# Performance work log

Measured on AMD Instinct MI355X. Metric: run time of the kernel, lower is better.

The kernel has to match this reference:

```python
import jax, jax.numpy as jnp
import numpy as np

HEADS = 4
DIM_HEAD = 32
SCALE = DIM_HEAD ** -0.5

# Energy conventions (Hopfield / Lagrangian formulation):
#  Neuron(x): g = activation(x); e = sum(x*g) - L(x)
#  Synapse(g, x): e = -sum(g*x)
#  identity Lagrangian: L(x) = 0.5*sum(x^2), g = x  => Conv2d block energy = -0.5*sum(x^2)
#  softmax Lagrangian: L(x) = sum(logsumexp(x, -1)), g = softmax(x, -1)

def setup_inputs() -> dict:
    key = jax.random.key(0)
    ks = jax.random.split(key, 5)
    b, c, h, w = 8, 256, 48, 48
    hidden = HEADS * DIM_HEAD  # 128
    return {
        "x": jax.random.normal(ks[0], (b, c, h, w), jnp.float32),
        "w_qkv": jax.random.normal(ks[1], (hidden * 3, c), jnp.float32) * 0.02,
        "b_qkv": jax.random.normal(ks[2], (hidden * 3,), jnp.float32) * 0.02,
        "w_out": jax.random.normal(ks[3], (c, hidden), jnp.float32) * 0.02,
        "b_out": jax.random.normal(ks[4], (c,), jnp.float32) * 0.02,
    }

def reference(x, w_qkv, b_qkv, w_out, b_out):
    b, c, h, w = x.shape
    # 1x1 conv == channel matmul
    qkv = jnp.einsum('oc,bcxy->boxy', w_qkv, x) + b_qkv[None, :, None, None]
    e_qkv = -0.5 * jnp.sum(qkv * qkv)  # identity-Lagrangian neuron + synapse energy
    q, k, v = jnp.split(qkv, 3, axis=1)
    # 'b (h c) x y -> b h c (x y)'
    def heads(t):
        return t.reshape(b, HEADS, DIM_HEAD, h * w)
    q, k, v = heads(q), heads(k), heads(v)
    q = q * SCALE
    sim = jnp.einsum('bhdi,bhdj->bhij', q, k)  # [b, heads, hw, hw]
    sim = sim - jax.lax.stop_gradient(jnp.max(sim, axis=-1, keepdims=True))
    attn = jax.nn.softmax(sim, axis=-1)
    # softmax-Lagrangian neuron energy: sum(sim*attn) - sum(logsumexp(sim, -1))
    e_attn = jnp.sum(sim * attn) - jnp.sum(jax.nn.logsumexp(sim, axis=-1))
    out = jnp.einsum('bhij,bhdj->bhid', attn, v)  # [b, heads, hw, dim_head]
    # 'b h (x y) d -> b (h d) x y'
    out = out.transpose(0, 1, 3, 2).reshape(b, HEADS * DIM_HEAD, h, w)
    out = jnp.einsum('oc,bcxy->boxy', w_out, out) + b_out[None, :, None, None]
    e_out = -0.5 * jnp.sum(out * out)
    return out, e_attn + e_out + e_qkv
```

## Files before the change

kernel.cpp:

```cpp
#include <hip/hip_runtime.h>
#include <hip/hip_bf16.h>

#define HW 2304
#define HW2 4608
#define NB 8
#define NC 256
#define HID 128
#define DH 32
#define NH 4
#define SCALE 0.17677669529663687f
#define LOG2E 1.4426950408889634f
#define LN2   0.6931471805599453f

#define NSPLIT 4
#define OSZ ((size_t)NB * HW * HID)

using bf16x8 = __attribute__((ext_vector_type(8))) short;
using f32x4  = __attribute__((ext_vector_type(4))) float;

__device__ __forceinline__ short f2bf(float f) {
    unsigned u = __float_as_uint(f);
    u += 0x7FFF + ((u >> 16) & 1);
    return (short)(u >> 16);
}
__device__ __forceinline__ float bf2f(short s) {
    return __uint_as_float(((unsigned)(unsigned short)s) << 16);
}
__device__ __forceinline__ unsigned pk2bf(float a, float b) {
    union { __hip_bfloat162 h; unsigned u; } cv;
    cv.h = __float22bfloat162_rn(float2{a, b});
    return cv.u;
}
__device__ __forceinline__ void gld16(const void* g, void* l) {
    __builtin_amdgcn_global_load_lds(
        (const __attribute__((address_space(1))) unsigned*)g,
        (__attribute__((address_space(3))) unsigned*)l, 16, 0, 0);
}
#define SB() __builtin_amdgcn_sched_barrier(0)

__global__ __launch_bounds__(256)
void prep(const float* __restrict__ x, const float* __restrict__ wq,
          const float* __restrict__ wo, short* __restrict__ Xt,
          short* __restrict__ Wq, short* __restrict__ Wo, float* __restrict__ wsz)
{
    if (blockIdx.z == 8) {
        const int bid = blockIdx.x + 36 * blockIdx.y;
        if (bid == 0 && threadIdx.x == 0) { wsz[0] = 0.f; ((int*)wsz)[1] = 0; }
        for (int i = bid * 256 + threadIdx.x; i < 384 * 256; i += 144 * 256) {
            Wq[i] = f2bf(wq[i]);
            if (i < 256 * 128) Wo[i] = f2bf(wo[i]);
        }
        return;
    }
    __shared__ short Tb[64][72];
    const int b = blockIdx.z, c0 = blockIdx.y * 64, s0 = blockIdx.x * 64;
    const int ts4 = (threadIdx.x & 15) * 4;
    const int cc0 = threadIdx.x >> 4;
    #pragma unroll
    for (int pp = 0; pp < 4; ++pp) {
        const int cc = cc0 + pp * 16;
        const float4 v = *(const float4*)(
            x + ((size_t)b * NC + c0 + cc) * HW + s0 + ts4);
        Tb[ts4 + 0][cc] = f2bf(v.x);
        Tb[ts4 + 1][cc] = f2bf(v.y);
        Tb[ts4 + 2][cc] = f2bf(v.z);
        Tb[ts4 + 3][cc] = f2bf(v.w);
    }
    __syncthreads();
    const int ss = threadIdx.x >> 2;
    const int c8 = (threadIdx.x & 3) * 8;
    #pragma unroll
    for (int pp = 0; pp < 2; ++pp) {
        const int cc = c8 + pp * 32;
        const bf16x8 v = *(const bf16x8*)&Tb[ss][cc];
        *(bf16x8*)(Xt + ((size_t)b * HW + s0 + ss) * NC + c0 + cc) = v;
    }
}

__global__ __launch_bounds__(256, 2)
void conv_qkv(const short* __restrict__ A, const short* __restrict__ Bt,
              const float* __restrict__ bias,
              short* __restrict__ Qb, short* __restrict__ Kb,
              short* __restrict__ Kt, short* __restrict__ Vb,
              float* __restrict__ E)
{
    constexpr int KD = NC;
    constexpr int NI = KD / 32;
    const int b  = blockIdx.z;
    const int bm = blockIdx.y * 64;
    const int bn = blockIdx.x * 128;
    const int t  = threadIdx.x;
    const int w  = t >> 6, lane = t & 63;
    const int n16 = lane & 15, quad = lane >> 4;

    __shared__ __align__(16) char csm[4 * 12288];
    __shared__ float red[4];

    const int rL = lane >> 2, cswz = (lane & 3) ^ (rL & 3);
    const char* agl = (const char*)(A  + (size_t)(bm + rL) * KD + cswz * 8);
    const char* bgl = (const char*)(Bt + ((size_t)b * HW + bn + rL) * KD + cswz * 8);

    auto issue = [&](int kc, int pbuf) {
        char* base = csm + pbuf * 12288;
        if (w == 0) {
            gld16(agl + (size_t)(0 * 16 * KD + kc) * 2, base + 0 * 1024);
            gld16(agl + (size_t)(1 * 16 * KD + kc) * 2, base + 1 * 1024);
            gld16(bgl + (size_t)(0 * 16 * KD + kc) * 2, base + 4096 + 0 * 1024);
        } else if (w == 1) {
            gld16(agl + (size_t)(2 * 16 * KD + kc) * 2, base + 2 * 1024);
            gld16(agl + (size_t)(3 * 16 * KD + kc) * 2, base + 3 * 1024);
            gld16(bgl + (size_t)(1 * 16 * KD + kc) * 2, base + 4096 + 1 * 1024);
        } else if (w == 2) {
            gld16(bgl + (size_t)(2 * 16 * KD + kc) * 2, base + 4096 + 2 * 1024);
            gld16(bgl + (size_t)(3 * 16 * KD + kc) * 2, base + 4096 + 3 * 1024);
            gld16(bgl + (size_t)(4 * 16 * KD + kc) * 2, base + 4096 + 4 * 1024);
        } else {
            gld16(bgl + (size_t)(5 * 16 * KD + kc) * 2, base + 4096 + 5 * 1024);
            gld16(bgl + (size_t)(6 * 16 * KD + kc) * 2, base + 4096 + 6 * 1024);
            gld16(bgl + (size_t)(7 * 16 * KD + kc) * 2, base + 4096 + 7 * 1024);
        }
    };

    f32x4 acc[4][2] = {};
    const int rsw = (quad ^ (n16 & 3)) * 16;

    issue(0, 0); SB();
    issue(32, 1); SB();
    for (int ki = 0; ki < NI; ++ki) {
        if (ki + 2 < NI) {
            issue((ki + 2) * 32, (ki + 2) & 3);
            asm volatile("s_waitcnt vmcnt(6)" ::: "memory");
        } else if (ki + 2 == NI) {
            asm volatile("s_waitcnt vmcnt(3)" ::: "memory");
        } else {
            asm volatile("s_waitcnt vmcnt(0)" ::: "memory");
        }
        __builtin_amdgcn_s_barrier();
        SB();

        const char* Ap = csm + (ki & 3) * 12288;
        const char* Bp = Ap + 4096;
        bf16x8 am[4], bq[2];
        #pragma unroll
        for (int tm = 0; tm < 4; ++tm)
            am[tm] = *(const bf16x8*)(Ap + tm * 1024 + n16 * 64 + rsw);
        #pragma unroll
        for (int j = 0; j < 2; ++j)
            bq[j] = *(const bf16x8*)(Bp + (w * 2 + j) * 1024 + n16 * 64 + rsw);
        #pragma unroll
        for (int tm = 0; tm < 4; ++tm)
            #pragma unroll
            for (int j = 0; j < 2; ++j)
                acc[tm][j] = __builtin_amdgcn_mfma_f32_16x16x32_bf16(am[tm], bq[j], acc[tm][j], 0, 0, 0);
    }

    float e = 0.f;
    #pragma unroll
    for (int tm = 0; tm < 4; ++tm) {
        const int o0 = bm + tm * 16 + quad * 4;
        const float4 bb = *(const float4*)(bias + o0);
        #pragma unroll
        for (int j = 0; j < 2; ++j) {
            const int s = bn + (w * 2 + j) * 16 + n16;
            float v[4] = {acc[tm][j][0] + bb.x, acc[tm][j][1] + bb.y,
                          acc[tm][j][2] + bb.z, acc[tm][j][3] + bb.w};
            e -= 0.5f * (v[0]*v[0] + v[1]*v[1] + v[2]*v[2] + v[3]*v[3]);
            if (o0 < HID) {
                const int h = o0 >> 5, dh0 = o0 & 31;
                const float qs = SCALE * LOG2E;
                short4 pk = {f2bf(v[0]*qs), f2bf(v[1]*qs),
                             f2bf(v[2]*qs), f2bf(v[3]*qs)};
                *(short4*)(Qb + ((size_t)(b * NH + h) * HW + s) * DH + dh0) = pk;
            } else if (o0 < 2 * HID) {
                const int c = o0 - HID, h = c >> 5, dh0 = c & 31;
                const int g = s & 31;
                const int sp = (s & ~31) | ((g & 4) << 2) | ((g >> 3) << 2) | (g & 3);
                short4 pk = {f2bf(v[0]), f2bf(v[1]), f2bf(v[2]), f2bf(v[3])};
                *(short4*)(Kb + ((size_t)(b * NH + h) * HW + sp) * DH + dh0) = pk;
                #pragma unroll
                for (int r = 0; r < 4; ++r)
                    Kt[((size_t)(b * NH + h) * DH + dh0 + r) * HW + s] = f2bf(v[r]);
            } else {
                const int c = o0 - 2 * HID, h = c >> 5, dh0 = c & 31;
                #pragma unroll
                for (int r = 0; r < 4; ++r)
                    Vb[((size_t)(b * NH + h) * DH + dh0 + r) * HW + s] = f2bf(v[r]);
            }
        }
    }

    #pragma unroll
    for (int off = 32; off > 0; off >>= 1) e += __shfl_down(e, off);
    if (lane == 0) red[w] = e;
    __syncthreads();
    if (t == 0) atomicAdd(E, red[0] + red[1] + red[2] + red[3]);
}

__global__ __launch_bounds__(256)
void flashsplit(const short* __restrict__ Qb, const short* __restrict__ Kb,
                const short* __restrict__ Kt, const short* __restrict__ Vb,
                short* __restrict__ Oh, float* __restrict__ lsP,
                float* __restrict__ tsP)
{
    __shared__ __align__(16) char smem[2 * 12288];

    constexpr int ITERS = HW / (NSPLIT * 64);
    const int bh   = blockIdx.y;
    const int kh   = blockIdx.z;
    const int w    = threadIdx.x >> 6;
    const int lane = threadIdx.x & 63;
    const int n16  = lane & 15, quad = lane >> 4;
    const int qb   = blockIdx.x * 128 + w * 32;
    const int key0 = kh * ITERS * 64;

    bf16x8 aq[2];
    #pragma unroll
    for (int qg = 0; qg < 2; ++qg)
        aq[qg] = *(const bf16x8*)(Qb + ((size_t)bh * HW + qb + qg * 16 + n16) * DH + quad * 8);
    SB();

    const int rL = lane >> 2, cL = (lane & 3) ^ (rL & 3);
    const char* Kglb  = (const char*)(Kb + (size_t)bh * HW * DH);
    const char* Vglb  = (const char*)(Vb + (size_t)bh * DH * HW);
    const char* Ktglb = (const char*)(Kt + (size_t)bh * DH * HW);
    const int pca  = w & 1;
    const int ktca = w >> 1;
    const int ktu  = w & 1;

    auto stage = [&](int it, int pbuf) {
        char* buf = smem + pbuf * 12288;
        const int k64 = key0 + it * 64;
        if (w < 2) {
            const char* kg = Kglb + (size_t)(k64 + pca * 32 + rL) * 64 + cL * 16;
            gld16(kg,        buf + pca * 6144 + 0);
            gld16(kg + 1024, buf + pca * 6144 + 1024);
        } else {
            const char* vg = Vglb + (size_t)rL * HW2 + (size_t)(k64 + pca * 32) * 2 + cL * 16;
            gld16(vg,             buf + pca * 6144 + 2048);
            gld16(vg + 16 * HW2,  buf + pca * 6144 + 3072);
        }
        const char* kt = Ktglb + (size_t)(ktu * 16 + rL) * HW2
                       + (size_t)(k64 + ktca * 32) * 2 + cL * 16;
        gld16(kt, buf + ktca * 6144 + 4096 + ktu * 1024);
    };

    stage(0, 0);
    SB();

    f32x4 acc[2][2] = {};
    f32x4 lsacc[2] = {};
    f32x4 tsacc[2][2] = {};
    const int swz = (quad ^ (n16 & 3)) * 8;
    const bf16x8 ones = {0x3F80, 0x3F80, 0x3F80, 0x3F80,
                         0x3F80, 0x3F80, 0x3F80, 0x3F80};

    for (int it = 0; it < ITERS; ++it) {
        const int p = it & 1;
        asm volatile("s_waitcnt vmcnt(0)" ::: "memory");
        __builtin_amdgcn_s_barrier();
        SB();
        if (it + 1 < ITERS) stage(it + 1, p ^ 1);

        const char* buf = smem + p * 12288;
        #pragma unroll
        for (int ca = 0; ca < 2; ++ca) {
            const short* cb = (const short*)(buf + ca * 6144);

            const bf16x8 bk0  = *(const bf16x8*)(cb +        n16 * 32 + swz);
            const bf16x8 bk1  = *(const bf16x8*)(cb + 512  + n16 * 32 + swz);
            const bf16x8 bv0  = *(const bf16x8*)(cb + 1024 + n16 * 32 + swz);
            const bf16x8 bv1  = *(const bf16x8*)(cb + 1536 + n16 * 32 + swz);
            const bf16x8 bkt0 = *(const bf16x8*)(cb + 2048 + n16 * 32 + swz);
            const bf16x8 bkt1 = *(const bf16x8*)(cb + 2560 + n16 * 32 + swz);

            #pragma unroll
            for (int qg = 0; qg < 2; ++qg) {
                f32x4 z = {};
                const f32x4 s0 = __builtin_amdgcn_mfma_f32_16x16x32_bf16(bk0, aq[qg], z, 0, 0, 0);
                const f32x4 s1 = __builtin_amdgcn_mfma_f32_16x16x32_bf16(bk1, aq[qg], z, 0, 0, 0);
                float e0[4], e1[4];
                #pragma unroll
                for (int r = 0; r < 4; ++r) {
                    e0[r] = __builtin_amdgcn_exp2f(s0[r]);
                    e1[r] = __builtin_amdgcn_exp2f(s1[r]);
                }
                union { bf16x8 v; unsigned u[4]; } pa;
                pa.u[0] = pk2bf(e0[0], e0[1]);
                pa.u[1] = pk2bf(e0[2], e0[3]);
                pa.u[2] = pk2bf(e1[0], e1[1]);
                pa.u[3] = pk2bf(e1[2], e1[3]);
                acc[qg][0]   = __builtin_amdgcn_mfma_f32_16x16x32_bf16(bv0,  pa.v, acc[qg][0], 0, 0, 0);
                acc[qg][1]   = __builtin_amdgcn_mfma_f32_16x16x32_bf16(bv1,  pa.v, acc[qg][1], 0, 0, 0);
                lsacc[qg]    = __builtin_amdgcn_mfma_f32_16x16x32_bf16(ones, pa.v, lsacc[qg], 0, 0, 0);
                tsacc[qg][0] = __builtin_amdgcn_mfma_f32_16x16x32_bf16(bkt0, pa.v, tsacc[qg][0], 0, 0, 0);
                tsacc[qg][1] = __builtin_amdgcn_mfma_f32_16x16x32_bf16(bkt1, pa.v, tsacc[qg][1], 0, 0, 0);
            }
        }
    }

    const int bb = bh >> 2, h = bh & 3;
    short* dst = Oh + (size_t)kh * OSZ;
    #pragma unroll
    for (int qg = 0; qg < 2; ++qg) {
        const int q = qb + qg * 16 + n16;
        const float L = lsacc[qg][0];
        const short4 qa = *(const short4*)(Qb + ((size_t)bh * HW + q) * DH + quad * 4);
        const short4 qc = *(const short4*)(Qb + ((size_t)bh * HW + q) * DH + 16 + quad * 4);
        float ts = bf2f(qa.x) * tsacc[qg][0][0] + bf2f(qa.y) * tsacc[qg][0][1]
                 + bf2f(qa.z) * tsacc[qg][0][2] + bf2f(qa.w) * tsacc[qg][0][3]
                 + bf2f(qc.x) * tsacc[qg][1][0] + bf2f(qc.y) * tsacc[qg][1][1]
                 + bf2f(qc.z) * tsacc[qg][1][2] + bf2f(qc.w) * tsacc[qg][1][3];
        ts += __shfl_xor(ts, 16);
        ts += __shfl_xor(ts, 32);

        const float invl = 1.f / L;
        short* ap = dst + ((size_t)bb * HW + q) * HID + h * 32;
        short4 pk0 = {f2bf(acc[qg][0][0] * invl), f2bf(acc[qg][0][1] * invl),
                      f2bf(acc[qg][0][2] * invl), f2bf(acc[qg][0][3] * invl)};
        short4 pk1 = {f2bf(acc[qg][1][0] * invl), f2bf(acc[qg][1][1] * invl),
                      f2bf(acc[qg][1][2] * invl), f2bf(acc[qg][1][3] * invl)};
        *(short4*)(ap + quad * 4)      = pk0;
        *(short4*)(ap + 16 + quad * 4) = pk1;
        if (quad == 0) {
            const size_t li = (size_t)(kh * 32 + bh) * HW + q;
            lsP[li] = L;
            tsP[li] = ts;
        }
    }
}

__global__ __launch_bounds__(256, 2)
void conv_out(const short* __restrict__ A, const short* __restrict__ Oh,
              const float* __restrict__ lsP, const float* __restrict__ tsP,
              const float* __restrict__ bias, float* __restrict__ out0,
              float* __restrict__ E, int* __restrict__ ticket, int nblocks,
              float* __restrict__ edst)
{
    constexpr int KD = HID;
    constexpr int NI = KD / 32;
    const int b  = blockIdx.z;
    const int bm = blockIdx.y * 64;
    const int bn = blockIdx.x * 128;
    const int t  = threadIdx.x;
    const int w  = t >> 6, lane = t & 63;
    const int n16 = lane & 15, quad = lane >> 4;

    __shared__ __align__(16) char csm[24576];
    __shared__ float red[4];

    const int rL = lane >> 2, cswz = (lane & 3) ^ (rL & 3);
    const char* agl = (const char*)(A + (size_t)(bm + rL) * KD + cswz * 8);

    auto issueA = [&](int kc, int pbuf) {
        char* base = csm + pbuf * 12288;
        if (w == 0) {
            gld16(agl + (size_t)(0 * 16 * KD + kc) * 2, base + 0 * 1024);
            gld16(agl + (size_t)(1 * 16 * KD + kc) * 2, base + 1 * 1024);
        } else if (w == 1) {
            gld16(agl + (size_t)(2 * 16 * KD + kc) * 2, base + 2 * 1024);
            gld16(agl + (size_t)(3 * 16 * KD + kc) * 2, base + 3 * 1024);
        }
    };

    auto loadB = [&](int ki, bf16x8 pk[2]) {
        const int kc = ki * 32;
        const int bh = b * NH + ki;
        #pragma unroll
        for (int d = 0; d < 2; ++d) {
            const int blk = w * 2 + d;
            const int q = bn + blk * 16 + rL;
            float Ls[NSPLIT], sum = 0.f;
            #pragma unroll
            for (int kh = 0; kh < NSPLIT; ++kh) {
                Ls[kh] = lsP[(size_t)(kh * 32 + bh) * HW + q];
                sum += Ls[kh];
            }
            const float inv = 1.f / sum;
            float vv[8] = {};
            #pragma unroll
            for (int kh = 0; kh < NSPLIT; ++kh) {
                const float wk = Ls[kh] * inv;
                const bf16x8 o = *(const bf16x8*)(Oh + (size_t)kh * OSZ
                                    + ((size_t)b * HW + q) * HID + kc + cswz * 8);
                #pragma unroll
                for (int j = 0; j < 8; ++j) vv[j] += wk * bf2f(o[j]);
            }
            union { bf16x8 v; unsigned u[4]; } c;
            #pragma unroll
            for (int i = 0; i < 4; ++i) c.u[i] = pk2bf(vv[2*i], vv[2*i+1]);
            pk[d] = c.v;
        }
    };
    auto writeB = [&](const bf16x8 pk[2], int pbuf) {
        char* base = csm + pbuf * 12288 + 4096;
        #pragma unroll
        for (int d = 0; d < 2; ++d) {
            const int blk = w * 2 + d;
            *(bf16x8*)(base + blk * 1024 + rL * 64 + (lane & 3) * 16) = pk[d];
        }
    };

    f32x4 acc[4][2] = {};
    const int rsw = (quad ^ (n16 & 3)) * 16;

    bf16x8 bpk[2];
    loadB(0, bpk);
    issueA(0, 0);
    writeB(bpk, 0);
    for (int ki = 0; ki < NI; ++ki) {
        const int p = ki & 1;
        __syncthreads();
        if (ki + 1 < NI) { loadB(ki + 1, bpk); issueA((ki + 1) * 32, p ^ 1); }

        const char* Ap = csm + p * 12288;
        const char* Bp = Ap + 4096;
        bf16x8 am[4], bq[2];
        #pragma unroll
        for (int tm = 0; tm < 4; ++tm)
            am[tm] = *(const bf16x8*)(Ap + tm * 1024 + n16 * 64 + rsw);
        #pragma unroll
        for (int j = 0; j < 2; ++j)
            bq[j] = *(const bf16x8*)(Bp + (w * 2 + j) * 1024 + n16 * 64 + rsw);
        #pragma unroll
        for (int tm = 0; tm < 4; ++tm)
            #pragma unroll
            for (int j = 0; j < 2; ++j)
                acc[tm][j] = __builtin_amdgcn_mfma_f32_16x16x32_bf16(am[tm], bq[j], acc[tm][j], 0, 0, 0);

        if (ki + 1 < NI) writeB(bpk, p ^ 1);
    }

    float e = 0.f;
    #pragma unroll
    for (int tm = 0; tm < 4; ++tm) {
        const int o0 = bm + tm * 16 + quad * 4;
        const float4 bb = *(const float4*)(bias + o0);
        #pragma unroll
        for (int j = 0; j < 2; ++j) {
            const int s = bn + (w * 2 + j) * 16 + n16;
            float v[4] = {acc[tm][j][0] + bb.x, acc[tm][j][1] + bb.y,
                          acc[tm][j][2] + bb.z, acc[tm][j][3] + bb.w};
            e -= 0.5f * (v[0]*v[0] + v[1]*v[1] + v[2]*v[2] + v[3]*v[3]);
            #pragma unroll
            for (int r = 0; r < 4; ++r)
                out0[((size_t)b * NC + o0 + r) * HW + s] = v[r];
        }
    }

    if (blockIdx.y == 0) {
        const int q = bn + (t & 127);
        #pragma unroll
        for (int jj = 0; jj < 2; ++jj) {
            const int h = (t >> 7) * 2 + jj;
            const int bh = b * NH + h;
            float L = 0.f, T = 0.f;
            #pragma unroll
            for (int kh = 0; kh < NSPLIT; ++kh) {
                L += lsP[(size_t)(kh * 32 + bh) * HW + q];
                T += tsP[(size_t)(kh * 32 + bh) * HW + q];
            }
            e += (LN2 * T) / L - __logf(L);
        }
    }

    #pragma unroll
    for (int off = 32; off > 0; off >>= 1) e += __shfl_down(e, off);
    if (lane == 0) red[w] = e;
    __syncthreads();
    if (t == 0) {
        atomicAdd(E, red[0] + red[1] + red[2] + red[3]);
        __threadfence();
        const int prev = atomicAdd(ticket, 1);
        if (prev == nblocks - 1) {
            __threadfence();
            edst[0] = atomicAdd(E, 0.f);
        }
    }
}

extern "C" void kernel_launch(void* const* d_in, const int* in_sizes, int n_in,
                              void* d_out, int out_size, void* d_ws, size_t ws_size,
                              hipStream_t stream) {
    const float* x     = (const float*)d_in[0];
    const float* w_qkv = (const float*)d_in[1];
    const float* b_qkv = (const float*)d_in[2];
    const float* w_out = (const float*)d_in[3];
    const float* b_out = (const float*)d_in[4];
    float* out = (float*)d_out;

    float* wsf    = (float*)d_ws;
    float* E      = wsf;
    int*   ticket = (int*)d_ws + 1;
    short* Xt   = (short*)(wsf + 16);
    short* Wq   = Xt + (size_t)NB * HW * NC;
    short* Wo   = Wq + 384 * 256;
    short* Qb   = Wo + 256 * 128;
    short* Kb   = Qb + (size_t)NB * NH * HW * DH;
    short* Ktb  = Kb + (size_t)NB * NH * HW * DH;
    short* Vb   = Ktb + (size_t)NB * NH * HW * DH;
    short* Oh   = Vb + (size_t)NB * NH * HW * DH;
    float* lsP  = (float*)(Oh + NSPLIT * OSZ);
    float* tsP  = lsP + NSPLIT * 32 * HW;

    prep<<<dim3(HW / 64, NC / 64, NB + 1), 256, 0, stream>>>(
        x, w_qkv, w_out, Xt, Wq, Wo, wsf);
    conv_qkv<<<dim3(18, 6, NB), 256, 0, stream>>>(
        Wq, Xt, b_qkv, Qb, Kb, Ktb, Vb, E);
    flashsplit<<<dim3(HW / 128, NB * NH, NSPLIT), 256, 0, stream>>>(
        Qb, Kb, Ktb, Vb, Oh, lsP, tsP);
    conv_out<<<dim3(18, 4, NB), 256, 0, stream>>>(
        Wo, Oh, lsP, tsP, b_out, out, E, ticket, 18 * 4 * NB,
        out + (size_t)NB * NC * HW);
}
```

Measured before the change: 192.9 us.

## Double-buffer 64-wide K chunks in QKV conv and remap flash blocks per XCD

The QKV projection kernel now stages 64-channel K chunks into two large shared buffers, replacing the four-deep 32-channel ring with finer vmcnt waits. It waits for all loads, then prefetches the next chunk after the barrier, giving fewer loop iterations and barriers in exchange for coarser overlap. The flash-attention split kernel remaps its flat block index so that consecutive blocks on the same XCD share a (batch·head, key-split) group, aiming to improve L2 reuse of K/V. The remap hardcodes grid dimensions (18×32×NSPLIT).

```diff
diff --git a/kernel.cpp b/kernel.cpp
--- a/kernel.cpp
+++ b/kernel.cpp
@@ -85,7 +85,7 @@
               float* __restrict__ E)
 {
     constexpr int KD = NC;
-    constexpr int NI = KD / 32;
+    constexpr int NI = KD / 64;
     const int b  = blockIdx.z;
     const int bm = blockIdx.y * 64;
     const int bn = blockIdx.x * 128;
@@ -93,15 +93,14 @@
     const int w  = t >> 6, lane = t & 63;
     const int n16 = lane & 15, quad = lane >> 4;
 
-    __shared__ __align__(16) char csm[4 * 12288];
+    __shared__ __align__(16) char csm[2 * 24576];
     __shared__ float red[4];
 
     const int rL = lane >> 2, cswz = (lane & 3) ^ (rL & 3);
     const char* agl = (const char*)(A  + (size_t)(bm + rL) * KD + cswz * 8);
     const char* bgl = (const char*)(Bt + ((size_t)b * HW + bn + rL) * KD + cswz * 8);
 
-    auto issue = [&](int kc, int pbuf) {
-        char* base = csm + pbuf * 12288;
+    auto issue32 = [&](int kc, char* base) {
         if (w == 0) {
             gld16(agl + (size_t)(0 * 16 * KD + kc) * 2, base + 0 * 1024);
             gld16(agl + (size_t)(1 * 16 * KD + kc) * 2, base + 1 * 1024);
@@ -120,38 +119,39 @@
             gld16(bgl + (size_t)(7 * 16 * KD + kc) * 2, base + 4096 + 7 * 1024);
         }
     };
+    auto stage = [&](int kc, int pbuf) {
+        issue32(kc,      csm + pbuf * 24576);
+        issue32(kc + 32, csm + pbuf * 24576 + 12288);
+    };
 
     f32x4 acc[4][2] = {};
     const int rsw = (quad ^ (n16 & 3)) * 16;
 
-    issue(0, 0); SB();
-    issue(32, 1); SB();
+    stage(0, 0); SB();
     for (int ki = 0; ki < NI; ++ki) {
-        if (ki + 2 < NI) {
-            issue((ki + 2) * 32, (ki + 2) & 3);
-            asm volatile("s_waitcnt vmcnt(6)" ::: "memory");
-        } else if (ki + 2 == NI) {
-            asm volatile("s_waitcnt vmcnt(3)" ::: "memory");
-        } else {
-            asm volatile("s_waitcnt vmcnt(0)" ::: "memory");
-        }
+        const int p = ki & 1;
+        asm volatile("s_waitcnt vmcnt(0)" ::: "memory");
         __builtin_amdgcn_s_barrier();
         SB();
-
-        const char* Ap = csm + (ki & 3) * 12288;
-        const char* Bp = Ap + 4096;
-        bf16x8 am[4], bq[2];
-        #pragma unroll
-        for (int tm = 0; tm < 4; ++tm)
-            am[tm] = *(const bf16x8*)(Ap + tm * 1024 + n16 * 64 + rsw);
-        #pragma unroll
-        for (int j = 0; j < 2; ++j)
-            bq[j] = *(const bf16x8*)(Bp + (w * 2 + j) * 1024 + n16 * 64 + rsw);
-        #pragma unroll
-        for (int tm = 0; tm < 4; ++tm)
+        if (ki + 1 < NI) stage((ki + 1) * 64, p ^ 1);
+
+        #pragma unroll
+        for (int su = 0; su < 2; ++su) {
+            const char* Ap = csm + p * 24576 + su * 12288;
+            const char* Bp = Ap + 4096;
+            bf16x8 am[4], bq[2];
+            #pragma unroll
+            for (int tm = 0; tm < 4; ++tm)
+                am[tm] = *(const bf16x8*)(Ap + tm * 1024 + n16 * 64 + rsw);
             #pragma unroll
             for (int j = 0; j < 2; ++j)
-                acc[tm][j] = __builtin_amdgcn_mfma_f32_16x16x32_bf16(am[tm], bq[j], acc[tm][j], 0, 0, 0);
+                bq[j] = *(const bf16x8*)(Bp + (w * 2 + j) * 1024 + n16 * 64 + rsw);
+            #pragma unroll
+            for (int tm = 0; tm < 4; ++tm)
+                #pragma unroll
+                for (int j = 0; j < 2; ++j)
+                    acc[tm][j] = __builtin_amdgcn_mfma_f32_16x16x32_bf16(am[tm], bq[j], acc[tm][j], 0, 0, 0);
+        }
     }
 
     float e = 0.f;
@@ -205,12 +205,16 @@
     __shared__ __align__(16) char smem[2 * 12288];
 
     constexpr int ITERS = HW / (NSPLIT * 64);
-    const int bh   = blockIdx.y;
-    const int kh   = blockIdx.z;
+    const int flat = blockIdx.x + 18 * (blockIdx.y + 32 * blockIdx.z);
+    const int xcd  = flat & 7, j = flat >> 3;
+    const int g    = xcd + 8 * (j / 18);
+    const int m    = j % 18;
+    const int bh   = g & 31;
+    const int kh   = g >> 5;
     const int w    = threadIdx.x >> 6;
     const int lane = threadIdx.x & 63;
     const int n16  = lane & 15, quad = lane >> 4;
-    const int qb   = blockIdx.x * 128 + w * 32;
+    const int qb   = m * 128 + w * 32;
     const int key0 = kh * ITERS * 64;
 
     bf16x8 aq[2];
```

After: 193.7 us. About the same (+0.4%).
